# Kernel tuning notes

Hardware: AMD Instinct MI355X
Metric: run time of the kernel (lower is better)

Reference implementation:

```python
import jax, jax.numpy as jnp
import numpy as np
from jax.ops import segment_sum

N_NODES = 100000
N_EDGES = 1600000
N_GRAPHS = 128


def setup_inputs() -> dict:
    key = jax.random.key(0)
    ks = jax.random.split(key, 16)
    x = jax.random.normal(ks[0], (N_NODES, 128), dtype=jnp.float32)
    edge_index = jax.random.randint(ks[1], (2, N_EDGES), 0, N_NODES, dtype=jnp.int64)
    batch = jnp.sort(jax.random.randint(ks[2], (N_NODES,), 0, N_GRAPHS, dtype=jnp.int64))
    def glorot(k, fan_in, fan_out):
        lim = (6.0 / (fan_in + fan_out)) ** 0.5
        return jax.random.uniform(k, (fan_in, fan_out), jnp.float32, -lim, lim)
    return {
        "x": x, "edge_index": edge_index, "batch": batch,
        "W1": glorot(ks[3], 128, 64), "b1": jnp.zeros((64,), jnp.float32),
        "W2": glorot(ks[4], 64, 64),  "b2": jnp.zeros((64,), jnp.float32),
        "W3": glorot(ks[5], 64, 64),  "b3": jnp.zeros((64,), jnp.float32),
        "W4": glorot(ks[6], 64, 64),  "b4": jnp.zeros((64,), jnp.float32),
        "Wl": glorot(ks[7], 64, 1),   "bl": jnp.zeros((1,), jnp.float32),
    }


def _gcn_layer(x, row, col, norm, W, b):
    # x: [N, Cin] -> [N, Cout]; gather source feats, scale, scatter-add at target
    h = x @ W                                 # dense transform first (GCNConv order)
    msg = norm[:, None] * h[row]              # [E, Cout]
    out = segment_sum(msg, col, num_segments=N_NODES)
    return out + b


def reference(x, edge_index, batch, W1, b1, W2, b2, W3, b3, W4, b4, Wl, bl):
    row, col = edge_index[0], edge_index[1]
    # symmetric degree normalization based on in-degree of col (PyG degree(col))
    deg = segment_sum(jnp.ones((N_EDGES,), x.dtype), col, num_segments=N_NODES)
    dinv = jnp.where(deg > 0, deg ** -0.5, jnp.zeros_like(deg))
    norm = dinv[row] * dinv[col]              # [E]

    h = _gcn_layer(x, row, col, norm, W1, b1)
    h = _gcn_layer(h, row, col, norm, W2, b2)
    h = _gcn_layer(h, row, col, norm, W3, b3)
    h = _gcn_layer(h, row, col, norm, W4, b4)  # [N, 64]

    # to_dense_batch + mean(dim=1): padded zeros count, so divide by max graph size
    sums = segment_sum(h, batch, num_segments=N_GRAPHS)          # [B, 64]
    counts = segment_sum(jnp.ones((N_NODES,), h.dtype), batch, num_segments=N_GRAPHS)
    n_max = jnp.max(counts)
    pooled = sums / n_max                                        # [B, 64]
    return pooled @ Wl + bl                                      # [B, 1]
```

## Files before the change

### kernel.cpp

```cpp
#include <hip/hip_runtime.h>
#include <hip/hip_bf16.h>
#include <hip/hip_fp16.h>

#define N_NODES 100000
#define N_EDGES 1600000
#define N_GRAPHS 128

#define BSH 9
#define BNODES 512
#define NB 196
#define CAP 12288
#define BLK 512
#define EPB (N_EDGES / BLK)
#define RECMAX 10240

#define SPLIT 4

typedef __attribute__((ext_vector_type(8))) _Float16 v8h;
typedef __attribute__((ext_vector_type(4))) float v4f;
typedef __attribute__((ext_vector_type(4))) int vi4;
typedef __attribute__((ext_vector_type(2))) int vi2;
typedef __attribute__((ext_vector_type(4))) float vf4;

__device__ __forceinline__ float2 h2f(int bits) {
    return __half22float2(__builtin_bit_cast(__half2, bits));
}

__device__ __forceinline__ v8h zero8h() {
    v8h z = {(_Float16)0, (_Float16)0, (_Float16)0, (_Float16)0,
             (_Float16)0, (_Float16)0, (_Float16)0, (_Float16)0};
    return z;
}


__global__ __launch_bounds__(256) void k_hist(const int* __restrict__ col,
                                              int* __restrict__ hist_t) {
    __shared__ int h[NB];
    const int t = threadIdx.x, b = blockIdx.x;
    for (int i = t; i < NB; i += 256) h[i] = 0;
    __syncthreads();
    const int e0 = b * EPB;
    for (int i = t; i < EPB; i += 256) atomicAdd(&h[col[e0 + i] >> BSH], 1);
    __syncthreads();
    for (int i = t; i < NB; i += 256) hist_t[i * BLK + b] = h[i];
}

__global__ __launch_bounds__(512) void k_cursors(const int* __restrict__ hist_t,
                                                 int* __restrict__ cursors,
                                                 int* __restrict__ bcnt) {
    __shared__ int s[BLK];
    const int t = threadIdx.x, bin = blockIdx.x;
    const int v = hist_t[bin * BLK + t];
    s[t] = v; __syncthreads();
    for (int off = 1; off < BLK; off <<= 1) {
        int a = (t >= off) ? s[t - off] : 0;
        __syncthreads(); s[t] += a; __syncthreads();
    }
    cursors[bin * BLK + t] = bin * CAP + s[t] - v;
    if (t == BLK - 1) bcnt[bin] = s[t];
}

__global__ __launch_bounds__(256) void k_mid(const int* __restrict__ row,
                                             const int* __restrict__ col,
                                             const int* __restrict__ cursors,
                                             int* __restrict__ bedges) {
    __shared__ int cur[NB];
    const int t = threadIdx.x, b = blockIdx.x;
    for (int i = t; i < NB; i += 256) cur[i] = cursors[i * BLK + b];
    __syncthreads();
    const int e0 = b * EPB;
    for (int i = t; i < EPB; i += 256) {
        const int c = col[e0 + i];
        const int r = row[e0 + i];
        const int pos = atomicAdd(&cur[c >> BSH], 1);
        bedges[pos] = r | ((c & (BNODES - 1)) << 17);
    }
}

__global__ __launch_bounds__(512) void k_build(const int* __restrict__ bedges,
                                               const int* __restrict__ bcnt,
                                               int* __restrict__ csr,
                                               int* __restrict__ offs,
                                               int* __restrict__ deg_c,
                                               float* __restrict__ dinv) {
    __shared__ int rec[RECMAX];
    __shared__ int deg[BNODES];
    __shared__ int offx[BNODES];
    __shared__ int cur[BNODES];
    const int t = threadIdx.x, bin = blockIdx.x;
    const int base = bin * CAP;
    const int cnt = bcnt[bin];
    const int vb = bin << BSH;
    const int nn = min(BNODES, N_NODES - vb);
    for (int i = t; i < cnt; i += 512) rec[i] = bedges[base + i];
    deg[t] = 0;
    __syncthreads();
    for (int i = t; i < cnt; i += 512) atomicAdd(&deg[(rec[i] >> 17) & (BNODES - 1)], 1);
    __syncthreads();
    const int d = (t < nn) ? deg[t] : 0;
    const int pd = (d + 7) & ~7;
    offx[t] = pd; __syncthreads();
    for (int off = 1; off < BNODES; off <<= 1) {
        int a = (t >= off) ? offx[t - off] : 0;
        __syncthreads(); offx[t] += a; __syncthreads();
    }
    const int myoff = offx[t] - pd;
    cur[t] = myoff;
    if (t < nn) {
        offs[vb + t] = base + myoff;
        deg_c[vb + t] = d;
        dinv[vb + t] = (d > 0) ? rsqrtf((float)d) : 0.0f;
        for (int j = d; j < pd; j++) csr[base + myoff + j] = N_NODES;
    }
    __syncthreads();
    for (int i = t; i < cnt; i += 512) {
        const int r = rec[i];
        const int pos = atomicAdd(&cur[(r >> 17) & (BNODES - 1)], 1);
        csr[base + pos] = r & 0x1FFFF;
    }
}


template <int CIN, typename TIN>
__global__ __launch_bounds__(256) void k_gemm(const TIN* __restrict__ X,
                                              const float* __restrict__ W,
                                              const float* __restrict__ dinv,
                                              __half* __restrict__ H16) {
    constexpr int SBK = CIN + 8;
    __shared__ __align__(16) _Float16 sBh[64 * SBK];
    __shared__ __align__(16) _Float16 sBl[64 * SBK];
    const int t = threadIdx.x;
    const int w = t >> 6, lane = t & 63;
    const int quad = lane >> 4, l16 = lane & 15;
    const int nb = blockIdx.x * 64;

    for (int i = t; i < CIN * 16; i += 256) {
        const int k = i >> 4, c4 = (i & 15) * 4;
        const float4 wv = *reinterpret_cast<const float4*>(W + (size_t)k * 64 + c4);
        const float wf[4] = {wv.x, wv.y, wv.z, wv.w};
        #pragma unroll
        for (int j = 0; j < 4; j++) {
            const _Float16 hi = (_Float16)wf[j];
            sBh[(c4 + j) * SBK + k] = hi;
            sBl[(c4 + j) * SBK + k] = (_Float16)(wf[j] - (float)hi);
        }
    }
    __syncthreads();

    const int gn = nb + w * 16 + l16;
    v4f acc[4] = {};

    #pragma unroll
    for (int k0 = 0; k0 < CIN; k0 += 32) {
        const int kb = k0 + quad * 8;
        v8h afr;
        if (gn < N_NODES) {
            if constexpr (sizeof(TIN) == 2) {
                afr = *reinterpret_cast<const v8h*>((const __half*)X + (size_t)gn * CIN + kb);
            } else {
                const float4 u0 = *reinterpret_cast<const float4*>((const float*)X + (size_t)gn * CIN + kb);
                const float4 u1 = *reinterpret_cast<const float4*>((const float*)X + (size_t)gn * CIN + kb + 4);
                afr[0] = (_Float16)u0.x; afr[1] = (_Float16)u0.y;
                afr[2] = (_Float16)u0.z; afr[3] = (_Float16)u0.w;
                afr[4] = (_Float16)u1.x; afr[5] = (_Float16)u1.y;
                afr[6] = (_Float16)u1.z; afr[7] = (_Float16)u1.w;
            }
        } else {
            afr = zero8h();
        }
        v8h bh[4], bl[4];
        #pragma unroll
        for (int nt = 0; nt < 4; nt++) {
            bh[nt] = *reinterpret_cast<const v8h*>(&sBh[(nt * 16 + l16) * SBK + kb]);
            bl[nt] = *reinterpret_cast<const v8h*>(&sBl[(nt * 16 + l16) * SBK + kb]);
        }
        #pragma unroll
        for (int nt = 0; nt < 4; nt++) {
            acc[nt] = __builtin_amdgcn_mfma_f32_16x16x32_f16(afr, bh[nt], acc[nt], 0, 0, 0);
            acc[nt] = __builtin_amdgcn_mfma_f32_16x16x32_f16(afr, bl[nt], acc[nt], 0, 0, 0);
        }
    }

    #pragma unroll
    for (int reg = 0; reg < 4; reg++) {
        const int node = nb + w * 16 + quad * 4 + reg;
        if (node < N_NODES) {
            const float dv = dinv[node];
            #pragma unroll
            for (int nt = 0; nt < 4; nt++)
                H16[(size_t)node * 64 + nt * 16 + l16] =
                    __float2half(acc[nt][reg] * dv);
        }
    }
}


template <typename TOUT>
__global__ __launch_bounds__(256) void k_prop(const __half* __restrict__ Hin,
                                              const int* __restrict__ csr,
                                              const int* __restrict__ offs,
                                              const int* __restrict__ deg_c,
                                              const float* __restrict__ dinv,
                                              const float* __restrict__ bias,
                                              TOUT* __restrict__ Hout) {
    const int wave = threadIdx.x >> 6, lane = threadIdx.x & 63;
    const int quad = lane >> 4;
    const int l = lane & 15;
    const int v = blockIdx.x * 16 + wave * 4 + quad;
    const int start = offs[v];
    const int cp = (deg_c[v] + 7) & ~7;
    const int* ep = csr + start;
    const __half* hb = Hin + l * 4;
    float a0 = 0.f, a1 = 0.f, a2 = 0.f, a3 = 0.f;
    for (int j = 0; j < cp; j += 8) {
        const vi4 q0 = __builtin_nontemporal_load(reinterpret_cast<const vi4*>(ep + j));
        const vi4 q1 = __builtin_nontemporal_load(reinterpret_cast<const vi4*>(ep + j + 4));
        const vi2 r0 = *reinterpret_cast<const vi2*>(hb + (size_t)q0.x * 64);
        const vi2 r1 = *reinterpret_cast<const vi2*>(hb + (size_t)q0.y * 64);
        const vi2 r2 = *reinterpret_cast<const vi2*>(hb + (size_t)q0.z * 64);
        const vi2 r3 = *reinterpret_cast<const vi2*>(hb + (size_t)q0.w * 64);
        const vi2 r4 = *reinterpret_cast<const vi2*>(hb + (size_t)q1.x * 64);
        const vi2 r5 = *reinterpret_cast<const vi2*>(hb + (size_t)q1.y * 64);
        const vi2 r6 = *reinterpret_cast<const vi2*>(hb + (size_t)q1.z * 64);
        const vi2 r7 = *reinterpret_cast<const vi2*>(hb + (size_t)q1.w * 64);
        #define ACC(r) { \
            const float2 u = h2f(r.x); \
            const float2 w2 = h2f(r.y); \
            a0 += u.x; a1 += u.y; a2 += w2.x; a3 += w2.y; }
        ACC(r0) ACC(r1) ACC(r2) ACC(r3) ACC(r4) ACC(r5) ACC(r6) ACC(r7)
        #undef ACC
    }
    const float dv = dinv[v];
    const float4 bs = *reinterpret_cast<const float4*>(bias + l * 4);
    const float o0 = dv * a0 + bs.x, o1 = dv * a1 + bs.y;
    const float o2 = dv * a2 + bs.z, o3 = dv * a3 + bs.w;
    if constexpr (sizeof(TOUT) == 2) {
        vi2 pk;
        pk.x = __builtin_bit_cast(int, __floats2half2_rn(o0, o1));
        pk.y = __builtin_bit_cast(int, __floats2half2_rn(o2, o3));
        *reinterpret_cast<vi2*>((__half*)Hout + (size_t)v * 64 + l * 4) = pk;
    } else {
        vf4 o; o.x = o0; o.y = o1; o.z = o2; o.w = o3;
        __builtin_nontemporal_store(o,
            reinterpret_cast<vf4*>((float*)Hout + (size_t)v * 64 + l * 4));
    }
}


__global__ __launch_bounds__(256) void k_pool(const float* __restrict__ H,
                                              const int* __restrict__ batch,
                                              float* __restrict__ partial) {
    const int g = blockIdx.x >> 2;
    const int s = blockIdx.x & (SPLIT - 1);
    int lo = 0, hi = N_NODES;
    while (lo < hi) { int m = (lo + hi) >> 1; if (batch[m] < g) lo = m + 1; else hi = m; }
    const int a = lo;
    lo = 0; hi = N_NODES;
    while (lo < hi) { int m = (lo + hi) >> 1; if (batch[m] < g + 1) lo = m + 1; else hi = m; }
    const int b = lo;

    const int wave = threadIdx.x >> 6, lane = threadIdx.x & 63;
    const int lane16 = s * 4 + wave;
    float ac0 = 0.f, ac1 = 0.f, ac2 = 0.f, ac3 = 0.f;
    int v = a + lane16;
    for (; v + 48 < b; v += 64) {
        ac0 += H[(size_t)v * 64 + lane];
        ac1 += H[(size_t)(v + 16) * 64 + lane];
        ac2 += H[(size_t)(v + 32) * 64 + lane];
        ac3 += H[(size_t)(v + 48) * 64 + lane];
    }
    for (; v < b; v += 16) ac0 += H[(size_t)v * 64 + lane];
    const float acc = (ac0 + ac1) + (ac2 + ac3);

    __shared__ float red[4][64];
    red[wave][lane] = acc;
    __syncthreads();
    if (wave == 0) {
        const float r = (red[0][lane] + red[1][lane]) + (red[2][lane] + red[3][lane]);
        partial[((size_t)s * N_GRAPHS + g) * 64 + lane] = r;
    }
}

__global__ void k_final(const float* __restrict__ partial, const int* __restrict__ batch,
                        const float* __restrict__ Wl, const float* __restrict__ bl,
                        float* __restrict__ out) {
    __shared__ int scnt[128];
    int t = threadIdx.x;
    int lo = 0, hi = N_NODES;
    while (lo < hi) { int mid = (lo + hi) >> 1; if (batch[mid] < t) lo = mid + 1; else hi = mid; }
    int a = lo;
    lo = 0; hi = N_NODES;
    while (lo < hi) { int mid = (lo + hi) >> 1; if (batch[mid] < t + 1) lo = mid + 1; else hi = mid; }
    scnt[t] = lo - a;
    __syncthreads();
    for (int off = 64; off > 0; off >>= 1) {
        if (t < off) scnt[t] = max(scnt[t], scnt[t + off]);
        __syncthreads();
    }
    const float nmax = (float)scnt[0];
    float s = 0.f;
    for (int c = 0; c < 64; c++) {
        float g = 0.f;
        #pragma unroll
        for (int p = 0; p < SPLIT; p++)
            g += partial[((size_t)p * N_GRAPHS + t) * 64 + c];
        s += g * Wl[c];
    }
    out[t] = s / nmax + bl[0];
}


extern "C" void kernel_launch(void* const* d_in, const int* in_sizes, int n_in,
                              void* d_out, int out_size, void* d_ws, size_t ws_size,
                              hipStream_t stream) {
    const float* x    = (const float*)d_in[0];
    const int*   ei   = (const int*)d_in[1];
    const int*   batch= (const int*)d_in[2];
    const float* W1 = (const float*)d_in[3];  const float* b1 = (const float*)d_in[4];
    const float* W2 = (const float*)d_in[5];  const float* b2 = (const float*)d_in[6];
    const float* W3 = (const float*)d_in[7];  const float* b3 = (const float*)d_in[8];
    const float* W4 = (const float*)d_in[9];  const float* b4 = (const float*)d_in[10];
    const float* Wl = (const float*)d_in[11]; const float* bl = (const float*)d_in[12];
    float* out = (float*)d_out;

    const int* row = ei;
    const int* col = ei + N_EDGES;

    char* ws = (char*)d_ws;
    size_t off = 0;
    auto alloc = [&](size_t bytes) {
        void* p = ws + off;
        off = (off + bytes + 255) & ~(size_t)255;
        return p;
    };
    int*    hist_t  = (int*)alloc((size_t)NB * BLK * 4);
    int*    cursors = (int*)alloc((size_t)NB * BLK * 4);
    int*    bcnt    = (int*)alloc(NB * 4);
    int*    bedges  = (int*)alloc((size_t)NB * CAP * 4);
    int*    csr     = bedges;
    int*    offs    = (int*)alloc(N_NODES * 4);
    int*    deg_c   = (int*)alloc(N_NODES * 4);
    float*  dinv    = (float*)alloc(N_NODES * 4);
    __half* h16     = (__half*)alloc((size_t)(N_NODES + 1) * 64 * 2);
    __half* h_c     = (__half*)alloc((size_t)N_NODES * 64 * 2);
    float*  h_b     = (float*)alloc((size_t)N_NODES * 64 * 4);
    float*  partial = (float*)alloc((size_t)SPLIT * N_GRAPHS * 64 * 4);

    (void)hipMemsetAsync(h16 + (size_t)N_NODES * 64, 0, 64 * 2, stream);

    k_hist<<<BLK, 256, 0, stream>>>(col, hist_t);
    k_cursors<<<NB, 512, 0, stream>>>(hist_t, cursors, bcnt);
    k_mid<<<BLK, 256, 0, stream>>>(row, col, cursors, bedges);
    k_build<<<NB, 512, 0, stream>>>(bedges, bcnt, csr, offs, deg_c, dinv);

    const int GB = (N_NODES + 63) / 64;
    const int PB = N_NODES / 16;

    k_gemm<128, float><<<GB, 256, 0, stream>>>(x, W1, dinv, h16);
    k_prop<__half><<<PB, 256, 0, stream>>>(h16, csr, offs, deg_c, dinv, b1, h_c);
    k_gemm<64, __half><<<GB, 256, 0, stream>>>(h_c, W2, dinv, h16);
    k_prop<__half><<<PB, 256, 0, stream>>>(h16, csr, offs, deg_c, dinv, b2, h_c);
    k_gemm<64, __half><<<GB, 256, 0, stream>>>(h_c, W3, dinv, h16);
    k_prop<__half><<<PB, 256, 0, stream>>>(h16, csr, offs, deg_c, dinv, b3, h_c);
    k_gemm<64, __half><<<GB, 256, 0, stream>>>(h_c, W4, dinv, h16);
    k_prop<float><<<PB, 256, 0, stream>>>(h16, csr, offs, deg_c, dinv, b4, h_b);

    k_pool<<<N_GRAPHS * SPLIT, 256, 0, stream>>>(h_b, batch, partial);
    k_final<<<1, 128, 0, stream>>>(partial, batch, Wl, bl, out);
}
```

Before: 378.2 us.

## Split feature matrices into two 32-column planes and propagate each plane separately

Feature buffers are stored as two planes of 32 columns each, node-major within each plane. The propagation kernel gets a second grid dimension, one per plane. Within a node, the two 8-lane halves each take alternate edges and are combined with a shuffle. The aim is to shrink the gathered working set per pass (a 64-byte row per neighbour) so it fits better in cache, at the cost of reading the CSR indices twice and launching twice as many blocks. The GEMM and pool kernels are updated to the planar layout.

```diff
diff --git a/kernel.cpp b/kernel.cpp
--- a/kernel.cpp
+++ b/kernel.cpp
@@ -15,6 +15,8 @@
 #define RECMAX 10240
 
 #define SPLIT 4
+
+#define HROWS (N_NODES + 8)
 
 typedef __attribute__((ext_vector_type(8))) _Float16 v8h;
 typedef __attribute__((ext_vector_type(4))) float v4f;
@@ -156,7 +158,9 @@
         v8h afr;
         if (gn < N_NODES) {
             if constexpr (sizeof(TIN) == 2) {
-                afr = *reinterpret_cast<const v8h*>((const __half*)X + (size_t)gn * CIN + kb);
+                const int hf = kb >> 5, kin = kb & 31;
+                afr = *reinterpret_cast<const v8h*>(
+                    (const __half*)X + ((size_t)hf * N_NODES + gn) * 32 + kin);
             } else {
                 const float4 u0 = *reinterpret_cast<const float4*>((const float*)X + (size_t)gn * CIN + kb);
                 const float4 u1 = *reinterpret_cast<const float4*>((const float*)X + (size_t)gn * CIN + kb + 4);
@@ -188,7 +192,7 @@
             const float dv = dinv[node];
             #pragma unroll
             for (int nt = 0; nt < 4; nt++)
-                H16[(size_t)node * 64 + nt * 16 + l16] =
+                H16[((size_t)(nt >> 1) * HROWS + node) * 32 + (nt & 1) * 16 + l16] =
                     __float2half(acc[nt][reg] * dv);
         }
     }
@@ -205,44 +209,52 @@
                                               TOUT* __restrict__ Hout) {
     const int wave = threadIdx.x >> 6, lane = threadIdx.x & 63;
     const int quad = lane >> 4;
-    const int l = lane & 15;
+    const int q = lane & 15;
+    const int cg = q & 7;
+    const int par = q >> 3;
+    const int p = blockIdx.y;
     const int v = blockIdx.x * 16 + wave * 4 + quad;
     const int start = offs[v];
     const int cp = (deg_c[v] + 7) & ~7;
     const int* ep = csr + start;
-    const __half* hb = Hin + l * 4;
+    const __half* hb = Hin + (size_t)p * HROWS * 32 + cg * 4;
     float a0 = 0.f, a1 = 0.f, a2 = 0.f, a3 = 0.f;
     for (int j = 0; j < cp; j += 8) {
         const vi4 q0 = __builtin_nontemporal_load(reinterpret_cast<const vi4*>(ep + j));
         const vi4 q1 = __builtin_nontemporal_load(reinterpret_cast<const vi4*>(ep + j + 4));
-        const vi2 r0 = *reinterpret_cast<const vi2*>(hb + (size_t)q0.x * 64);
-        const vi2 r1 = *reinterpret_cast<const vi2*>(hb + (size_t)q0.y * 64);
-        const vi2 r2 = *reinterpret_cast<const vi2*>(hb + (size_t)q0.z * 64);
-        const vi2 r3 = *reinterpret_cast<const vi2*>(hb + (size_t)q0.w * 64);
-        const vi2 r4 = *reinterpret_cast<const vi2*>(hb + (size_t)q1.x * 64);
-        const vi2 r5 = *reinterpret_cast<const vi2*>(hb + (size_t)q1.y * 64);
-        const vi2 r6 = *reinterpret_cast<const vi2*>(hb + (size_t)q1.z * 64);
-        const vi2 r7 = *reinterpret_cast<const vi2*>(hb + (size_t)q1.w * 64);
+        const int ea = par ? q0.y : q0.x;
+        const int eb = par ? q0.w : q0.z;
+        const int ec = par ? q1.y : q1.x;
+        const int ed = par ? q1.w : q1.z;
+        const vi2 r0 = *reinterpret_cast<const vi2*>(hb + (size_t)ea * 32);
+        const vi2 r1 = *reinterpret_cast<const vi2*>(hb + (size_t)eb * 32);
+        const vi2 r2 = *reinterpret_cast<const vi2*>(hb + (size_t)ec * 32);
+        const vi2 r3 = *reinterpret_cast<const vi2*>(hb + (size_t)ed * 32);
         #define ACC(r) { \
             const float2 u = h2f(r.x); \
             const float2 w2 = h2f(r.y); \
             a0 += u.x; a1 += u.y; a2 += w2.x; a3 += w2.y; }
-        ACC(r0) ACC(r1) ACC(r2) ACC(r3) ACC(r4) ACC(r5) ACC(r6) ACC(r7)
+        ACC(r0) ACC(r1) ACC(r2) ACC(r3)
         #undef ACC
     }
-    const float dv = dinv[v];
-    const float4 bs = *reinterpret_cast<const float4*>(bias + l * 4);
-    const float o0 = dv * a0 + bs.x, o1 = dv * a1 + bs.y;
-    const float o2 = dv * a2 + bs.z, o3 = dv * a3 + bs.w;
-    if constexpr (sizeof(TOUT) == 2) {
-        vi2 pk;
-        pk.x = __builtin_bit_cast(int, __floats2half2_rn(o0, o1));
-        pk.y = __builtin_bit_cast(int, __floats2half2_rn(o2, o3));
-        *reinterpret_cast<vi2*>((__half*)Hout + (size_t)v * 64 + l * 4) = pk;
-    } else {
-        vf4 o; o.x = o0; o.y = o1; o.z = o2; o.w = o3;
-        __builtin_nontemporal_store(o,
-            reinterpret_cast<vf4*>((float*)Hout + (size_t)v * 64 + l * 4));
+    a0 += __shfl_xor(a0, 8); a1 += __shfl_xor(a1, 8);
+    a2 += __shfl_xor(a2, 8); a3 += __shfl_xor(a3, 8);
+    if (par == 0) {
+        const float dv = dinv[v];
+        const float4 bs = *reinterpret_cast<const float4*>(bias + p * 32 + cg * 4);
+        const float o0 = dv * a0 + bs.x, o1 = dv * a1 + bs.y;
+        const float o2 = dv * a2 + bs.z, o3 = dv * a3 + bs.w;
+        if constexpr (sizeof(TOUT) == 2) {
+            vi2 pk;
+            pk.x = __builtin_bit_cast(int, __floats2half2_rn(o0, o1));
+            pk.y = __builtin_bit_cast(int, __floats2half2_rn(o2, o3));
+            __builtin_nontemporal_store(pk,
+                reinterpret_cast<vi2*>((__half*)Hout + ((size_t)p * N_NODES + v) * 32 + cg * 4));
+        } else {
+            vf4 o; o.x = o0; o.y = o1; o.z = o2; o.w = o3;
+            __builtin_nontemporal_store(o,
+                reinterpret_cast<vf4*>((float*)Hout + ((size_t)p * N_NODES + v) * 32 + cg * 4));
+        }
     }
 }
 
@@ -261,15 +273,16 @@
 
     const int wave = threadIdx.x >> 6, lane = threadIdx.x & 63;
     const int lane16 = s * 4 + wave;
+    const size_t sbase = (size_t)(lane >> 5) * ((size_t)N_NODES * 32) + (lane & 31);
     float ac0 = 0.f, ac1 = 0.f, ac2 = 0.f, ac3 = 0.f;
     int v = a + lane16;
     for (; v + 48 < b; v += 64) {
-        ac0 += H[(size_t)v * 64 + lane];
-        ac1 += H[(size_t)(v + 16) * 64 + lane];
-        ac2 += H[(size_t)(v + 32) * 64 + lane];
-        ac3 += H[(size_t)(v + 48) * 64 + lane];
-    }
-    for (; v < b; v += 16) ac0 += H[(size_t)v * 64 + lane];
+        ac0 += H[sbase + (size_t)v * 32];
+        ac1 += H[sbase + (size_t)(v + 16) * 32];
+        ac2 += H[sbase + (size_t)(v + 32) * 32];
+        ac3 += H[sbase + (size_t)(v + 48) * 32];
+    }
+    for (; v < b; v += 16) ac0 += H[sbase + (size_t)v * 32];
     const float acc = (ac0 + ac1) + (ac2 + ac3);
 
     __shared__ float red[4][64];
@@ -341,12 +354,13 @@
     int*    offs    = (int*)alloc(N_NODES * 4);
     int*    deg_c   = (int*)alloc(N_NODES * 4);
     float*  dinv    = (float*)alloc(N_NODES * 4);
-    __half* h16     = (__half*)alloc((size_t)(N_NODES + 1) * 64 * 2);
-    __half* h_c     = (__half*)alloc((size_t)N_NODES * 64 * 2);
-    float*  h_b     = (float*)alloc((size_t)N_NODES * 64 * 4);
+    __half* h16     = (__half*)alloc((size_t)2 * HROWS * 32 * 2);
+    __half* h_c     = (__half*)alloc((size_t)2 * N_NODES * 32 * 2);
+    float*  h_b     = (float*)alloc((size_t)2 * N_NODES * 32 * 4);
     float*  partial = (float*)alloc((size_t)SPLIT * N_GRAPHS * 64 * 4);
 
-    (void)hipMemsetAsync(h16 + (size_t)N_NODES * 64, 0, 64 * 2, stream);
+    (void)hipMemsetAsync(h16 + ((size_t)0 * HROWS + N_NODES) * 32, 0, 32 * 2, stream);
+    (void)hipMemsetAsync(h16 + ((size_t)1 * HROWS + N_NODES) * 32, 0, 32 * 2, stream);
 
     k_hist<<<BLK, 256, 0, stream>>>(col, hist_t);
     k_cursors<<<NB, 512, 0, stream>>>(hist_t, cursors, bcnt);
@@ -354,16 +368,16 @@
     k_build<<<NB, 512, 0, stream>>>(bedges, bcnt, csr, offs, deg_c, dinv);
 
     const int GB = (N_NODES + 63) / 64;
-    const int PB = N_NODES / 16;
+    const dim3 gprop(N_NODES / 16, 2);
 
     k_gemm<128, float><<<GB, 256, 0, stream>>>(x, W1, dinv, h16);
-    k_prop<__half><<<PB, 256, 0, stream>>>(h16, csr, offs, deg_c, dinv, b1, h_c);
+    k_prop<__half><<<gprop, 256, 0, stream>>>(h16, csr, offs, deg_c, dinv, b1, h_c);
     k_gemm<64, __half><<<GB, 256, 0, stream>>>(h_c, W2, dinv, h16);
-    k_prop<__half><<<PB, 256, 0, stream>>>(h16, csr, offs, deg_c, dinv, b2, h_c);
+    k_prop<__half><<<gprop, 256, 0, stream>>>(h16, csr, offs, deg_c, dinv, b2, h_c);
     k_gemm<64, __half><<<GB, 256, 0, stream>>>(h_c, W3, dinv, h16);
-    k_prop<__half><<<PB, 256, 0, stream>>>(h16, csr, offs, deg_c, dinv, b3, h_c);
+    k_prop<__half><<<gprop, 256, 0, stream>>>(h16, csr, offs, deg_c, dinv, b3, h_c);
     k_gemm<64, __half><<<GB, 256, 0, stream>>>(h_c, W4, dinv, h16);
-    k_prop<float><<<PB, 256, 0, stream>>>(h16, csr, offs, deg_c, dinv, b4, h_b);
+    k_prop<float><<<gprop, 256, 0, stream>>>(h16, csr, offs, deg_c, dinv, b4, h_b);
 
     k_pool<<<N_GRAPHS * SPLIT, 256, 0, stream>>>(h_b, batch, partial);
     k_final<<<1, 128, 0, stream>>>(partial, batch, Wl, bl, out);
```

Result: slower. 430.2 us (+13.8%).

## Widen prop gathers to 16B with edge-parity split, fold memset, parallelize final

Applied to the files above, without the earlier changes.

The propagation kernel now has each lane gather 8 halves (16 bytes) per neighbor row. Even and odd edges are split across two half-groups, whose partial sums are combined with an xor shuffle before one half writes the output. This cuts the number of gather instructions per edge while keeping the same lanes per node. The padding-row memset is folded into the histogram kernel, dropping one API call. The final reduction now runs one block per graph with wave shuffles instead of a single serial block. The risk is extra shuffle work and half the lanes sitting idle during the epilogue.

```diff
diff --git a/kernel.cpp b/kernel.cpp
--- a/kernel.cpp
+++ b/kernel.cpp
@@ -34,9 +34,12 @@
 
 
 __global__ __launch_bounds__(256) void k_hist(const int* __restrict__ col,
-                                              int* __restrict__ hist_t) {
+                                              int* __restrict__ hist_t,
+                                              __half* __restrict__ h16) {
     __shared__ int h[NB];
     const int t = threadIdx.x, b = blockIdx.x;
+    if (b == 0 && t < 64)
+        h16[(size_t)N_NODES * 64 + t] = __float2half(0.0f);
     for (int i = t; i < NB; i += 256) h[i] = 0;
     __syncthreads();
     const int e0 = b * EPB;
@@ -205,44 +208,61 @@
                                               TOUT* __restrict__ Hout) {
     const int wave = threadIdx.x >> 6, lane = threadIdx.x & 63;
     const int quad = lane >> 4;
-    const int l = lane & 15;
+    const int par = (lane >> 3) & 1;
+    const int cl = lane & 7;
     const int v = blockIdx.x * 16 + wave * 4 + quad;
     const int start = offs[v];
     const int cp = (deg_c[v] + 7) & ~7;
     const int* ep = csr + start;
-    const __half* hb = Hin + l * 4;
+    const __half* hb = Hin + cl * 8;
     float a0 = 0.f, a1 = 0.f, a2 = 0.f, a3 = 0.f;
+    float a4 = 0.f, a5 = 0.f, a6 = 0.f, a7 = 0.f;
     for (int j = 0; j < cp; j += 8) {
         const vi4 q0 = __builtin_nontemporal_load(reinterpret_cast<const vi4*>(ep + j));
         const vi4 q1 = __builtin_nontemporal_load(reinterpret_cast<const vi4*>(ep + j + 4));
-        const vi2 r0 = *reinterpret_cast<const vi2*>(hb + (size_t)q0.x * 64);
-        const vi2 r1 = *reinterpret_cast<const vi2*>(hb + (size_t)q0.y * 64);
-        const vi2 r2 = *reinterpret_cast<const vi2*>(hb + (size_t)q0.z * 64);
-        const vi2 r3 = *reinterpret_cast<const vi2*>(hb + (size_t)q0.w * 64);
-        const vi2 r4 = *reinterpret_cast<const vi2*>(hb + (size_t)q1.x * 64);
-        const vi2 r5 = *reinterpret_cast<const vi2*>(hb + (size_t)q1.y * 64);
-        const vi2 r6 = *reinterpret_cast<const vi2*>(hb + (size_t)q1.z * 64);
-        const vi2 r7 = *reinterpret_cast<const vi2*>(hb + (size_t)q1.w * 64);
+        const int ea = par ? q0.y : q0.x;
+        const int eb = par ? q0.w : q0.z;
+        const int ec = par ? q1.y : q1.x;
+        const int ed = par ? q1.w : q1.z;
+        const vi4 r0 = *reinterpret_cast<const vi4*>(hb + (size_t)ea * 64);
+        const vi4 r1 = *reinterpret_cast<const vi4*>(hb + (size_t)eb * 64);
+        const vi4 r2 = *reinterpret_cast<const vi4*>(hb + (size_t)ec * 64);
+        const vi4 r3 = *reinterpret_cast<const vi4*>(hb + (size_t)ed * 64);
         #define ACC(r) { \
-            const float2 u = h2f(r.x); \
-            const float2 w2 = h2f(r.y); \
-            a0 += u.x; a1 += u.y; a2 += w2.x; a3 += w2.y; }
-        ACC(r0) ACC(r1) ACC(r2) ACC(r3) ACC(r4) ACC(r5) ACC(r6) ACC(r7)
+            const float2 u0 = h2f(r.x), u1 = h2f(r.y); \
+            const float2 u2 = h2f(r.z), u3 = h2f(r.w); \
+            a0 += u0.x; a1 += u0.y; a2 += u1.x; a3 += u1.y; \
+            a4 += u2.x; a5 += u2.y; a6 += u3.x; a7 += u3.y; }
+        ACC(r0) ACC(r1) ACC(r2) ACC(r3)
         #undef ACC
     }
-    const float dv = dinv[v];
-    const float4 bs = *reinterpret_cast<const float4*>(bias + l * 4);
-    const float o0 = dv * a0 + bs.x, o1 = dv * a1 + bs.y;
-    const float o2 = dv * a2 + bs.z, o3 = dv * a3 + bs.w;
-    if constexpr (sizeof(TOUT) == 2) {
-        vi2 pk;
-        pk.x = __builtin_bit_cast(int, __floats2half2_rn(o0, o1));
-        pk.y = __builtin_bit_cast(int, __floats2half2_rn(o2, o3));
-        *reinterpret_cast<vi2*>((__half*)Hout + (size_t)v * 64 + l * 4) = pk;
-    } else {
-        vf4 o; o.x = o0; o.y = o1; o.z = o2; o.w = o3;
-        __builtin_nontemporal_store(o,
-            reinterpret_cast<vf4*>((float*)Hout + (size_t)v * 64 + l * 4));
+    a0 += __shfl_xor(a0, 8); a1 += __shfl_xor(a1, 8);
+    a2 += __shfl_xor(a2, 8); a3 += __shfl_xor(a3, 8);
+    a4 += __shfl_xor(a4, 8); a5 += __shfl_xor(a5, 8);
+    a6 += __shfl_xor(a6, 8); a7 += __shfl_xor(a7, 8);
+    if (par == 0) {
+        const float dv = dinv[v];
+        const float4 b0 = *reinterpret_cast<const float4*>(bias + cl * 8);
+        const float4 b1 = *reinterpret_cast<const float4*>(bias + cl * 8 + 4);
+        const float o0 = dv * a0 + b0.x, o1 = dv * a1 + b0.y;
+        const float o2 = dv * a2 + b0.z, o3 = dv * a3 + b0.w;
+        const float o4 = dv * a4 + b1.x, o5 = dv * a5 + b1.y;
+        const float o6 = dv * a6 + b1.z, o7 = dv * a7 + b1.w;
+        if constexpr (sizeof(TOUT) == 2) {
+            vi4 pk;
+            pk.x = __builtin_bit_cast(int, __floats2half2_rn(o0, o1));
+            pk.y = __builtin_bit_cast(int, __floats2half2_rn(o2, o3));
+            pk.z = __builtin_bit_cast(int, __floats2half2_rn(o4, o5));
+            pk.w = __builtin_bit_cast(int, __floats2half2_rn(o6, o7));
+            __builtin_nontemporal_store(pk,
+                reinterpret_cast<vi4*>((__half*)Hout + (size_t)v * 64 + cl * 8));
+        } else {
+            vf4 olo; olo.x = o0; olo.y = o1; olo.z = o2; olo.w = o3;
+            vf4 ohi; ohi.x = o4; ohi.y = o5; ohi.z = o6; ohi.w = o7;
+            float* dst = (float*)Hout + (size_t)v * 64 + cl * 8;
+            __builtin_nontemporal_store(olo, reinterpret_cast<vf4*>(dst));
+            __builtin_nontemporal_store(ohi, reinterpret_cast<vf4*>(dst + 4));
+        }
     }
 }
 
@@ -281,32 +301,35 @@
     }
 }
 
-__global__ void k_final(const float* __restrict__ partial, const int* __restrict__ batch,
-                        const float* __restrict__ Wl, const float* __restrict__ bl,
-                        float* __restrict__ out) {
-    __shared__ int scnt[128];
-    int t = threadIdx.x;
-    int lo = 0, hi = N_NODES;
-    while (lo < hi) { int mid = (lo + hi) >> 1; if (batch[mid] < t) lo = mid + 1; else hi = mid; }
-    int a = lo;
-    lo = 0; hi = N_NODES;
-    while (lo < hi) { int mid = (lo + hi) >> 1; if (batch[mid] < t + 1) lo = mid + 1; else hi = mid; }
-    scnt[t] = lo - a;
-    __syncthreads();
-    for (int off = 64; off > 0; off >>= 1) {
-        if (t < off) scnt[t] = max(scnt[t], scnt[t + off]);
-        __syncthreads();
-    }
-    const float nmax = (float)scnt[0];
+__global__ __launch_bounds__(64) void k_final(const float* __restrict__ partial,
+                                              const int* __restrict__ batch,
+                                              const float* __restrict__ Wl,
+                                              const float* __restrict__ bl,
+                                              float* __restrict__ out) {
+    const int g = blockIdx.x, lane = threadIdx.x;
+    int m = 0;
+    #pragma unroll
+    for (int h = 0; h < 2; h++) {
+        const int gg = lane + h * 64;
+        int lo = 0, hi = N_NODES;
+        while (lo < hi) { int mid = (lo + hi) >> 1; if (batch[mid] < gg) lo = mid + 1; else hi = mid; }
+        const int a = lo;
+        lo = 0; hi = N_NODES;
+        while (lo < hi) { int mid = (lo + hi) >> 1; if (batch[mid] < gg + 1) lo = mid + 1; else hi = mid; }
+        m = max(m, lo - a);
+    }
+    #pragma unroll
+    for (int off = 32; off > 0; off >>= 1) m = max(m, __shfl_xor(m, off));
+    const float nmax = (float)m;
+
     float s = 0.f;
-    for (int c = 0; c < 64; c++) {
-        float g = 0.f;
-        #pragma unroll
-        for (int p = 0; p < SPLIT; p++)
-            g += partial[((size_t)p * N_GRAPHS + t) * 64 + c];
-        s += g * Wl[c];
-    }
-    out[t] = s / nmax + bl[0];
+    #pragma unroll
+    for (int p = 0; p < SPLIT; p++)
+        s += partial[((size_t)p * N_GRAPHS + g) * 64 + lane];
+    s *= Wl[lane];
+    #pragma unroll
+    for (int off = 32; off > 0; off >>= 1) s += __shfl_xor(s, off);
+    if (lane == 0) out[g] = s / nmax + bl[0];
 }
 
 
@@ -346,9 +369,7 @@
     float*  h_b     = (float*)alloc((size_t)N_NODES * 64 * 4);
     float*  partial = (float*)alloc((size_t)SPLIT * N_GRAPHS * 64 * 4);
 
-    (void)hipMemsetAsync(h16 + (size_t)N_NODES * 64, 0, 64 * 2, stream);
-
-    k_hist<<<BLK, 256, 0, stream>>>(col, hist_t);
+    k_hist<<<BLK, 256, 0, stream>>>(col, hist_t, h16);
     k_cursors<<<NB, 512, 0, stream>>>(hist_t, cursors, bcnt);
     k_mid<<<BLK, 256, 0, stream>>>(row, col, cursors, bedges);
     k_build<<<NB, 512, 0, stream>>>(bedges, bcnt, csr, offs, deg_c, dinv);
@@ -366,5 +387,5 @@
     k_prop<float><<<PB, 256, 0, stream>>>(h16, csr, offs, deg_c, dinv, b4, h_b);
 
     k_pool<<<N_GRAPHS * SPLIT, 256, 0, stream>>>(h_b, batch, partial);
-    k_final<<<1, 128, 0, stream>>>(partial, batch, Wl, bl, out);
-}
+    k_final<<<N_GRAPHS, 64, 0, stream>>>(partial, batch, Wl, bl, out);
+}
```

Measured after the change: 364.2 us. -3.7%, faster.
